# Kernel optimization log

Hardware: AMD Instinct MI355X
Metric: run time of the kernel (lower is better)

Reference implementation:

```python
import jax, jax.numpy as jnp
import numpy as np

B, S, DIM = 2, 2048, 2048
NH, HD, HDR = 16, 128, 64
DCKV, DCQ = 512, 1536


def _lin(x, W, b):
    return x @ W.T + b


def _rotate_half(x):
    x1, x2 = jnp.split(x, 2, axis=-1)
    return jnp.concatenate([-x2, x1], axis=-1)


def _rope(x, cos, sin):
    # x: [..., s, hdr]; cos/sin: [s, hdr]
    return x * cos + _rotate_half(x) * sin


def setup_inputs() -> dict:
    key = jax.random.key(0)
    ks = jax.random.split(key, 20)
    sc = 0.02

    def w(k, shape):
        return (jax.random.normal(k, shape, jnp.float32) * sc)

    inp = {}
    inp['x'] = jax.random.normal(ks[0], (B, S, DIM), jnp.float32)
    # standard RoPE tables for the decoupled rotary dim
    inv_freq = 1.0 / (10000.0 ** (jnp.arange(0, HDR, 2, dtype=jnp.float32) / HDR))
    t = jnp.arange(S, dtype=jnp.float32)
    freqs = jnp.outer(t, inv_freq)                      # [S, HDR/2]
    emb = jnp.concatenate([freqs, freqs], axis=-1)      # [S, HDR]
    inp['freq_cos'] = jnp.cos(emb)
    inp['freq_sin'] = jnp.sin(emb)
    inp['W_dq'] = w(ks[1], (DCQ, DIM));  inp['b_dq'] = jnp.zeros((DCQ,), jnp.float32)
    inp['W_uq'] = w(ks[2], (NH * HD, DCQ)); inp['b_uq'] = jnp.zeros((NH * HD,), jnp.float32)
    inp['W_qr'] = w(ks[3], (NH * HDR, DCQ)); inp['b_qr'] = jnp.zeros((NH * HDR,), jnp.float32)
    inp['W_dkv'] = w(ks[4], (DCKV, DIM)); inp['b_dkv'] = jnp.zeros((DCKV,), jnp.float32)
    inp['W_uk'] = w(ks[5], (NH * HD, DCKV)); inp['b_uk'] = jnp.zeros((NH * HD,), jnp.float32)
    inp['W_uv'] = w(ks[6], (NH * HD, DCKV)); inp['b_uv'] = jnp.zeros((NH * HD,), jnp.float32)
    inp['W_kr'] = w(ks[7], (HDR, DIM)); inp['b_kr'] = jnp.zeros((HDR,), jnp.float32)
    inp['W_out'] = w(ks[8], (DIM, DIM)); inp['b_out'] = jnp.zeros((DIM,), jnp.float32)
    return inp


def reference(x, freq_cos, freq_sin,
              W_dq, b_dq, W_uq, b_uq, W_qr, b_qr,
              W_dkv, b_dkv, W_uk, b_uk, W_uv, b_uv,
              W_kr, b_kr, W_out, b_out):
    b, s, d = x.shape
    c_q = _lin(x, W_dq, b_dq)                                  # [b,s,dcq]
    c_kv = _lin(x, W_dkv, b_dkv)                               # [b,s,dckv]
    c_q_r = _lin(c_q, W_qr, b_qr).reshape(b, s, NH, HDR).transpose(0, 2, 1, 3)  # [b,nh,s,hdr]
    k_r = _lin(x, W_kr, b_kr)[:, None]                         # [b,1,s,hdr]
    cos = freq_cos[:s]
    sin = freq_sin[:s]
    r_q = _rope(c_q_r, cos, sin)
    r_k = _rope(k_r, cos, sin)
    r_q = r_q.transpose(0, 2, 1, 3).reshape(b, s, NH * HDR)    # [b,s,nh*hdr]
    r_k = r_k[:, 0]                                            # [b,s,hdr]
    q = jnp.concatenate([_lin(c_q, W_uq, b_uq), r_q], axis=-1)  # [b,s,nh*hd+nh*hdr]
    k_base = _lin(c_kv, W_uk, b_uk)                            # [b,s,nh*hd]
    v = _lin(c_kv, W_uv, b_uv)                                 # [b,s,nh*hd]
    r_k_exp = jnp.broadcast_to(r_k[:, :, None, :], (b, s, NH, HDR)).reshape(b, s, NH * HDR)
    k = jnp.concatenate([k_base, r_k_exp], axis=-1)
    # faithful to original: view the concat into nh chunks of (hd+hdr)
    q = q.reshape(b, s, NH, HD + HDR).transpose(0, 2, 1, 3)    # [b,nh,s,hd+hdr]
    k = k.reshape(b, s, NH, HD + HDR).transpose(0, 2, 1, 3)
    v = v.reshape(b, s, NH, HD).transpose(0, 2, 1, 3)          # [b,nh,s,hd]
    scale = 1.0 / np.float32(np.sqrt(HD + HDR))
    att = jnp.einsum('bhqd,bhkd->bhqk', q, k) * scale          # [b,nh,s,s]
    mask = jnp.tril(jnp.ones((s, s), dtype=bool))
    att = jnp.where(mask, att, jnp.float32(-jnp.inf))
    att = jax.nn.softmax(att, axis=-1)
    y = jnp.einsum('bhqk,bhkd->bhqd', att, v)                  # [b,nh,s,hd]
    y = y.transpose(0, 2, 1, 3).reshape(b, s, d)
    return _lin(y, W_out, b_out)
```

## Files before the change

### kernel.cpp

```cpp
#include <hip/hip_runtime.h>
#include <hip/hip_bf16.h>
#include <stdint.h>


typedef __bf16 bf16x8 __attribute__((ext_vector_type(8)));
typedef float  f32x4  __attribute__((ext_vector_type(4)));

__device__ __forceinline__ uint16_t f2bf(float f) {
    uint32_t u = __builtin_bit_cast(uint32_t, f);
    u = (u + 0x7FFFu + ((u >> 16) & 1u)) >> 16;
    return (uint16_t)u;
}
__device__ __forceinline__ float bf2f(uint16_t h) {
    uint32_t u = ((uint32_t)h) << 16;
    return __builtin_bit_cast(float, u);
}

typedef __attribute__((address_space(3))) uint32_t lds_u32_t;
typedef const __attribute__((address_space(1))) uint32_t glb_u32_t;

__device__ __forceinline__ void gld16(const void* g, const void* l) {
    __builtin_amdgcn_global_load_lds((glb_u32_t*)(uintptr_t)g,
                                     (lds_u32_t*)(uint32_t)(uintptr_t)l, 16, 0, 0);
}

__global__ __launch_bounds__(256)
void conv_kernel(const float* __restrict__ src, uint16_t* __restrict__ dst,
                 int n_src, int n_dst)
{
    int i = (blockIdx.x * 256 + threadIdx.x) << 2;
    if (i >= n_dst) return;
    ushort4 o;
    if (i < n_src) {
        float4 v = *(const float4*)(src + i);
        o.x = f2bf(v.x); o.y = f2bf(v.y); o.z = f2bf(v.z); o.w = f2bf(v.w);
    } else {
        o.x = 0; o.y = 0; o.z = 0; o.w = 0;
    }
    *(ushort4*)(dst + i) = o;
}

template<int MODE>
__global__ __launch_bounds__(256, 2)
void gemm_fused(const uint16_t* __restrict__ A, const uint16_t* __restrict__ W,
                const float* __restrict__ b0, const float* __restrict__ b1,
                const float* __restrict__ b2,
                void* __restrict__ O0, void* __restrict__ O1,
                int M, int N, int K, int lda, int s1, int s2)
{
    __shared__ __align__(16) uint16_t Alds[128 * 32];
    __shared__ __align__(16) uint16_t Blds[128 * 32];

    const int tid  = threadIdx.x;
    const int lane = tid & 63;
    const int wave = tid >> 6;
    const int wm   = wave >> 1;
    const int wn   = wave & 1;
    const int m0   = blockIdx.y << 7;
    const int n0   = blockIdx.x << 7;

    f32x4 acc[4][4];
    #pragma unroll
    for (int i = 0; i < 4; ++i)
        #pragma unroll
        for (int j = 0; j < 4; ++j)
            acc[i][j] = (f32x4){0.f, 0.f, 0.f, 0.f};

    const int r0 = (wave << 5) + (lane >> 2);
    const int ck = (lane & 3) << 3;
    const uint16_t* gA0 = A + (size_t)(m0 + r0) * lda + ck;
    const uint16_t* gA1 = gA0 + (size_t)16 * lda;
    const uint16_t* gB0 = W + (size_t)(n0 + r0) * K + ck;
    const uint16_t* gB1 = gB0 + (size_t)16 * K;
    const uint16_t* lA0 = Alds + (wave << 10);
    const uint16_t* lA1 = lA0 + 512;
    const uint16_t* lB0 = Blds + (wave << 10);
    const uint16_t* lB1 = lB0 + 512;

    const int rsel = lane & 15;
    const int g8   = (lane >> 4) << 3;

    const int nK = K >> 5;
    for (int kt = 0; kt < nK; ++kt) {
        __syncthreads();
        gld16(gA0, lA0); gld16(gA1, lA1);
        gld16(gB0, lB0); gld16(gB1, lB1);
        gA0 += 32; gA1 += 32; gB0 += 32; gB1 += 32;
        __syncthreads();

        bf16x8 af[4], bfr[4];
        #pragma unroll
        for (int i = 0; i < 4; ++i)
            af[i] = *(const bf16x8*)&Alds[(((wm << 6) + (i << 4) + rsel) << 5) + g8];
        #pragma unroll
        for (int j = 0; j < 4; ++j)
            bfr[j] = *(const bf16x8*)&Blds[(((wn << 6) + (j << 4) + rsel) << 5) + g8];

        #pragma unroll
        for (int i = 0; i < 4; ++i)
            #pragma unroll
            for (int j = 0; j < 4; ++j)
                acc[i][j] = __builtin_amdgcn_mfma_f32_16x16x32_bf16(af[i], bfr[j], acc[i][j], 0, 0, 0);
    }

    const int col = lane & 15;
    const int rg  = lane >> 4;
    #pragma unroll
    for (int i = 0; i < 4; ++i) {
        #pragma unroll
        for (int j = 0; j < 4; ++j) {
            int n = n0 + (wn << 6) + (j << 4) + col;
            if (n >= N) continue;
            float bv = (n < s1) ? b0[n] : (n < s2) ? b1[n - s1] : b2[n - s2];
            float v[4];
            #pragma unroll
            for (int r = 0; r < 4; ++r) v[r] = acc[i][j][r] + bv;
            int mbase = m0 + (wm << 6) + (i << 4) + (rg << 2);
            if (MODE == 0) {
                uint16_t* o = (uint16_t*)O0 + (size_t)mbase * N + n;
                #pragma unroll
                for (int r = 0; r < 4; ++r) o[(size_t)r * N] = f2bf(v[r]);
            } else if (MODE == 3) {
                float* o = (float*)O0 + (size_t)mbase * N + n;
                #pragma unroll
                for (int r = 0; r < 4; ++r) o[(size_t)r * N] = v[r];
            } else {
                if (n < s1) {
                    int hh = n / 192, d = n - hh * 192;
                    int b = mbase >> 11, s = mbase & 2047;
                    uint16_t* o = (uint16_t*)O0 + (((size_t)(b * 16 + hh) * 2048 + s) * 192) + d;
                    #pragma unroll
                    for (int r = 0; r < 4; ++r) o[r * 192] = f2bf(v[r]);
                } else if (MODE == 4) {
                    int nn = n - s1;
                    uint16_t* o = (uint16_t*)O1 + (size_t)mbase * (N - s1) + nn;
                    #pragma unroll
                    for (int r = 0; r < 4; ++r) o[(size_t)r * (N - s1)] = f2bf(v[r]);
                } else {
                    int nn = n - s1;
                    int hh = nn >> 7, d = nn & 127;
                    int b = mbase >> 11, s = mbase & 2047;
                    ushort4 o4;
                    o4.x = f2bf(v[0]); o4.y = f2bf(v[1]); o4.z = f2bf(v[2]); o4.w = f2bf(v[3]);
                    *(ushort4*)&((uint16_t*)O1)[(((size_t)(b * 16 + hh) * 128 + d) * 2048) + s] = o4;
                }
            }
        }
    }
}

__global__ __launch_bounds__(256)
void rope_q_kernel(const uint16_t* __restrict__ raw, const float* __restrict__ fc,
                   const float* __restrict__ fs, uint16_t* __restrict__ qp)
{
    int gid = blockIdx.x * 256 + threadIdx.x;
    int m = gid >> 10, n = gid & 1023;
    int hh = n >> 6, d = n & 63;
    int b = m >> 11, s = m & 2047;
    float x  = bf2f(raw[(size_t)m * 1024 + n]);
    float xo = bf2f(raw[(size_t)m * 1024 + hh * 64 + ((d < 32) ? d + 32 : d - 32)]);
    float rot = (d < 32) ? -xo : xo;
    float v = x * fc[s * 64 + d] + rot * fs[s * 64 + d];
    int f = 2048 + n;
    int head = f / 192, dq = f - head * 192;
    qp[(((size_t)(b * 16 + head) * 2048 + s) * 192) + dq] = f2bf(v);
}

__global__ __launch_bounds__(256)
void rope_k_kernel(const uint16_t* __restrict__ raw, int ldr,
                   const float* __restrict__ fc, const float* __restrict__ fs,
                   uint16_t* __restrict__ kp)
{
    int gid = blockIdx.x * 256 + threadIdx.x;
    int m = gid >> 6, d = gid & 63;
    int b = m >> 11, s = m & 2047;
    float x  = bf2f(raw[(size_t)m * ldr + d]);
    float xo = bf2f(raw[(size_t)m * ldr + ((d < 32) ? d + 32 : d - 32)]);
    float rot = (d < 32) ? -xo : xo;
    uint16_t bv = f2bf(x * fc[s * 64 + d] + rot * fs[s * 64 + d]);
    #pragma unroll
    for (int hh = 0; hh < 16; ++hh) {
        int f = 2048 + hh * 64 + d;
        int head = f / 192, dk = f - head * 192;
        kp[(((size_t)(b * 16 + head) * 2048 + s) * 192) + dk] = bv;
    }
}

__global__ __launch_bounds__(256)
void attn_mfma3(const uint16_t* __restrict__ qp, const uint16_t* __restrict__ kp,
                const uint16_t* __restrict__ vt, uint16_t* __restrict__ yf)
{
    __shared__ uint16_t Ks[64][200];
    __shared__ uint16_t Vs[128][72];
    __shared__ uint16_t Ps[4][16][72];

    const int tid  = threadIdx.x;
    const int lane = tid & 63;
    const int w    = tid >> 6;
    const int g    = lane >> 4;
    const int li   = lane & 15;
    const int bh   = blockIdx.y;
    const int b    = bh >> 4;
    const int h    = bh & 15;

    const size_t qkb = (size_t)bh * 2048 * 192;
    const size_t vtb = (size_t)bh * 128 * 2048;
    const float scl = 0.07216878364870323f * 1.4426950408889634f;

    for (int pass = 0; pass < 2; ++pass) {
        const int jq = pass ? (int)blockIdx.x : 31 - (int)blockIdx.x;
        const int q0 = jq << 6;

        bf16x8 qf[6];
        #pragma unroll
        for (int kk = 0; kk < 6; ++kk)
            qf[kk] = *(const bf16x8*)(qp + qkb +
                (size_t)(q0 + (w << 4) + li) * 192 + kk * 32 + (g << 3));

        float mst[4], lst[4];
        f32x4 oacc[8];
        #pragma unroll
        for (int r = 0; r < 4; ++r) { mst[r] = -__builtin_inff(); lst[r] = 0.f; }
        #pragma unroll
        for (int ct = 0; ct < 8; ++ct) oacc[ct] = (f32x4){0.f, 0.f, 0.f, 0.f};

        for (int t = 0; t <= jq; ++t) {
            const int j0 = t << 6;
            __syncthreads();
            #pragma unroll
            for (int p = 0; p < 6; ++p) {
                int idx = tid + p * 256;
                int r = idx / 24, c8 = (idx - r * 24) << 3;
                *(bf16x8*)&Ks[r][c8] = *(const bf16x8*)(kp + qkb + (size_t)(j0 + r) * 192 + c8);
            }
            #pragma unroll
            for (int p = 0; p < 8; ++p) {
                int idx = tid + p * 256;
                int r = idx >> 4, c4 = (idx & 15) << 2;
                *(ushort4*)&Vs[r][c4] = *(const ushort4*)(vt + vtb + (size_t)r * 2048 + j0 + c4);
            }
            __syncthreads();

            f32x4 sacc[4];
            #pragma unroll
            for (int c = 0; c < 4; ++c) sacc[c] = (f32x4){0.f, 0.f, 0.f, 0.f};
            #pragma unroll
            for (int c = 0; c < 4; ++c) {
                #pragma unroll
                for (int kk = 0; kk < 6; ++kk) {
                    bf16x8 kf = *(const bf16x8*)&Ks[(c << 4) + li][kk * 32 + (g << 3)];
                    sacc[c] = __builtin_amdgcn_mfma_f32_16x16x32_bf16(qf[kk], kf, sacc[c], 0, 0, 0);
                }
            }

            float corr[4];
            #pragma unroll
            for (int r = 0; r < 4; ++r) {
                const int rq = q0 + (w << 4) + (g << 2) + r;
                float sv[4];
                float mx = -__builtin_inff();
                #pragma unroll
                for (int c = 0; c < 4; ++c) {
                    int colk = j0 + (c << 4) + li;
                    sv[c] = (colk <= rq) ? sacc[c][r] * scl : -__builtin_inff();
                    mx = fmaxf(mx, sv[c]);
                }
                #pragma unroll
                for (int off = 8; off >= 1; off >>= 1) mx = fmaxf(mx, __shfl_xor(mx, off, 64));
                float mnew = fmaxf(mst[r], mx);
                corr[r] = exp2f(mst[r] - mnew);
                mst[r] = mnew;
                float psum = 0.f;
                #pragma unroll
                for (int c = 0; c < 4; ++c) {
                    float p = exp2f(sv[c] - mnew);
                    psum += p;
                    Ps[w][(g << 2) + r][(c << 4) + li] = f2bf(p);
                }
                #pragma unroll
                for (int off = 8; off >= 1; off >>= 1) psum += __shfl_xor(psum, off, 64);
                lst[r] = lst[r] * corr[r] + psum;
            }

            #pragma unroll
            for (int ct = 0; ct < 8; ++ct)
                #pragma unroll
                for (int r = 0; r < 4; ++r) oacc[ct][r] *= corr[r];

            bf16x8 pf0 = *(const bf16x8*)&Ps[w][li][(g << 3)];
            bf16x8 pf1 = *(const bf16x8*)&Ps[w][li][32 + (g << 3)];
            #pragma unroll
            for (int ct = 0; ct < 8; ++ct) {
                bf16x8 vf0 = *(const bf16x8*)&Vs[(ct << 4) + li][(g << 3)];
                bf16x8 vf1 = *(const bf16x8*)&Vs[(ct << 4) + li][32 + (g << 3)];
                oacc[ct] = __builtin_amdgcn_mfma_f32_16x16x32_bf16(pf0, vf0, oacc[ct], 0, 0, 0);
                oacc[ct] = __builtin_amdgcn_mfma_f32_16x16x32_bf16(pf1, vf1, oacc[ct], 0, 0, 0);
            }
        }

        #pragma unroll
        for (int r = 0; r < 4; ++r) {
            float inv = 1.f / lst[r];
            int rq = q0 + (w << 4) + (g << 2) + r;
            size_t obase = ((size_t)(b * 2048 + rq) * 2048) + h * 128;
            #pragma unroll
            for (int ct = 0; ct < 8; ++ct)
                yf[obase + (ct << 4) + li] = f2bf(oacc[ct][r] * inv);
        }
    }
}

extern "C" void kernel_launch(void* const* d_in, const int* in_sizes, int n_in,
                              void* d_out, int out_size, void* d_ws, size_t ws_size,
                              hipStream_t stream)
{
    const float* x     = (const float*)d_in[0];
    const float* fcos  = (const float*)d_in[1];
    const float* fsin  = (const float*)d_in[2];
    const float* W_dq  = (const float*)d_in[3];
    const float* b_dq  = (const float*)d_in[4];
    const float* W_uq  = (const float*)d_in[5];
    const float* b_uq  = (const float*)d_in[6];
    const float* W_qr  = (const float*)d_in[7];
    const float* b_qr  = (const float*)d_in[8];
    const float* W_dkv = (const float*)d_in[9];
    const float* b_dkv = (const float*)d_in[10];
    const float* W_uk  = (const float*)d_in[11];
    const float* b_uk  = (const float*)d_in[12];
    const float* W_uv  = (const float*)d_in[13];
    const float* b_uv  = (const float*)d_in[14];
    const float* W_kr  = (const float*)d_in[15];
    const float* b_kr  = (const float*)d_in[16];
    const float* W_out = (const float*)d_in[17];
    const float* b_out = (const float*)d_in[18];

    char* ws = (char*)d_ws;
    uint16_t* xb     = (uint16_t*)(ws + 0);
    uint16_t* Wcat2  = (uint16_t*)(ws + 0);
    uint16_t* Wcat3  = (uint16_t*)(ws + 9437184);
    uint16_t* yf     = (uint16_t*)(ws + 0);
    uint16_t* Wout_b = (uint16_t*)(ws + 16777216);
    uint16_t* qp     = (uint16_t*)(ws + 25165824);
    uint16_t* kp     = (uint16_t*)(ws + 50331648);
    uint16_t* qr_raw = (uint16_t*)(ws + 50331648);
    uint16_t* vt     = (uint16_t*)(ws + 75497472);
    uint16_t* Wcat1  = (uint16_t*)(ws + 75497472);
    uint16_t* c_all  = (uint16_t*)(ws + 92274688);

    dim3 blk(256);
    conv_kernel<<<dim3(8192), blk, 0, stream>>>(x,     xb,                8388608, 8388608);
    conv_kernel<<<dim3(3072), blk, 0, stream>>>(W_dq,  Wcat1,             3145728, 3145728);
    conv_kernel<<<dim3(1024), blk, 0, stream>>>(W_dkv, Wcat1 + 3145728,   1048576, 1048576);
    conv_kernel<<<dim3( 256), blk, 0, stream>>>(W_kr,  Wcat1 + 4194304,    131072,  262144);
    conv_kernel<<<dim3(4096), blk, 0, stream>>>(W_out, Wout_b,            4194304, 4194304);

    gemm_fused<0><<<dim3(17, 32), blk, 0, stream>>>(
        xb, Wcat1, b_dq, b_dkv, b_kr, c_all, nullptr,
        4096, 2112, 2048, 2048, 1536, 2048);

    conv_kernel<<<dim3(3072), blk, 0, stream>>>(W_uq, Wcat2,             3145728, 3145728);
    conv_kernel<<<dim3(1536), blk, 0, stream>>>(W_qr, Wcat2 + 3145728,   1572864, 1572864);
    conv_kernel<<<dim3(1024), blk, 0, stream>>>(W_uk, Wcat3,             1048576, 1048576);
    conv_kernel<<<dim3(1024), blk, 0, stream>>>(W_uv, Wcat3 + 1048576,   1048576, 1048576);

    gemm_fused<4><<<dim3(24, 32), blk, 0, stream>>>(
        c_all, Wcat2, b_uq, b_qr, b_qr, qp, qr_raw,
        4096, 3072, 1536, 2112, 2048, 3072);

    rope_q_kernel<<<dim3(16384), blk, 0, stream>>>(qr_raw, fcos, fsin, qp);

    gemm_fused<5><<<dim3(32, 32), blk, 0, stream>>>(
        c_all + 1536, Wcat3, b_uk, b_uv, b_uv, kp, vt,
        4096, 4096, 512, 2112, 2048, 4096);

    rope_k_kernel<<<dim3(1024), blk, 0, stream>>>(c_all + 2048, 2112, fcos, fsin, kp);

    attn_mfma3<<<dim3(16, 32), blk, 0, stream>>>(qp, kp, vt, yf);

    gemm_fused<3><<<dim3(16, 32), blk, 0, stream>>>(
        yf, Wout_b, b_out, b_out, b_out, d_out, nullptr,
        4096, 2048, 2048, 2048, 2048, 2048);
}
```

Before: 362.2 us.

## Fuse q RoPE into up-projection epilogue and flatten attention grid to one tile per block

Applies the q rotary embedding directly in the MODE 4 GEMM epilogue, taking the partner element from the accumulator tile j^2, which removes the separate rope_q kernel and its intermediate buffer round trip. The attention kernel now launches 1024 blocks, each handling a single query tile, ordered from the longest causal tile down. Previously 512 blocks each paired a long and a short tile. This gives the scheduler finer load balancing but loses the explicit pairing, and the epilogue now does extra loads from the cos/sin tables.

```diff
diff --git a/kernel.cpp b/kernel.cpp
--- a/kernel.cpp
+++ b/kernel.cpp
@@ -45,6 +45,7 @@
 void gemm_fused(const uint16_t* __restrict__ A, const uint16_t* __restrict__ W,
                 const float* __restrict__ b0, const float* __restrict__ b1,
                 const float* __restrict__ b2,
+                const float* __restrict__ fc, const float* __restrict__ fs,
                 void* __restrict__ O0, void* __restrict__ O1,
                 int M, int N, int K, int lda, int s1, int s2)
 {
@@ -125,21 +126,30 @@
                 #pragma unroll
                 for (int r = 0; r < 4; ++r) o[(size_t)r * N] = v[r];
             } else {
+                int b = mbase >> 11, s = mbase & 2047;
                 if (n < s1) {
                     int hh = n / 192, d = n - hh * 192;
-                    int b = mbase >> 11, s = mbase & 2047;
                     uint16_t* o = (uint16_t*)O0 + (((size_t)(b * 16 + hh) * 2048 + s) * 192) + d;
                     #pragma unroll
                     for (int r = 0; r < 4; ++r) o[r * 192] = f2bf(v[r]);
                 } else if (MODE == 4) {
                     int nn = n - s1;
-                    uint16_t* o = (uint16_t*)O1 + (size_t)mbase * (N - s1) + nn;
+                    int d  = nn & 63;
+                    float bp = b1[nn ^ 32];
+                    int f = 2048 + nn;
+                    int head = f / 192, dq = f - head * 192;
+                    uint16_t* o = (uint16_t*)O0 + (((size_t)(b * 16 + head) * 2048 + s) * 192) + dq;
                     #pragma unroll
-                    for (int r = 0; r < 4; ++r) o[(size_t)r * (N - s1)] = f2bf(v[r]);
+                    for (int r = 0; r < 4; ++r) {
+                        float pv  = acc[i][j ^ 2][r] + bp;
+                        float rot = (d < 32) ? -pv : pv;
+                        int   sl  = s + r;
+                        float out = v[r] * fc[(size_t)sl * 64 + d] + rot * fs[(size_t)sl * 64 + d];
+                        o[r * 192] = f2bf(out);
+                    }
                 } else {
                     int nn = n - s1;
                     int hh = nn >> 7, d = nn & 127;
-                    int b = mbase >> 11, s = mbase & 2047;
                     ushort4 o4;
                     o4.x = f2bf(v[0]); o4.y = f2bf(v[1]); o4.z = f2bf(v[2]); o4.w = f2bf(v[3]);
                     *(ushort4*)&((uint16_t*)O1)[(((size_t)(b * 16 + hh) * 128 + d) * 2048) + s] = o4;
@@ -147,23 +157,6 @@
             }
         }
     }
-}
-
-__global__ __launch_bounds__(256)
-void rope_q_kernel(const uint16_t* __restrict__ raw, const float* __restrict__ fc,
-                   const float* __restrict__ fs, uint16_t* __restrict__ qp)
-{
-    int gid = blockIdx.x * 256 + threadIdx.x;
-    int m = gid >> 10, n = gid & 1023;
-    int hh = n >> 6, d = n & 63;
-    int b = m >> 11, s = m & 2047;
-    float x  = bf2f(raw[(size_t)m * 1024 + n]);
-    float xo = bf2f(raw[(size_t)m * 1024 + hh * 64 + ((d < 32) ? d + 32 : d - 32)]);
-    float rot = (d < 32) ? -xo : xo;
-    float v = x * fc[s * 64 + d] + rot * fs[s * 64 + d];
-    int f = 2048 + n;
-    int head = f / 192, dq = f - head * 192;
-    qp[(((size_t)(b * 16 + head) * 2048 + s) * 192) + dq] = f2bf(v);
 }
 
 __global__ __launch_bounds__(256)
@@ -187,7 +180,7 @@
 }
 
 __global__ __launch_bounds__(256)
-void attn_mfma3(const uint16_t* __restrict__ qp, const uint16_t* __restrict__ kp,
+void attn_mfma5(const uint16_t* __restrict__ qp, const uint16_t* __restrict__ kp,
                 const uint16_t* __restrict__ vt, uint16_t* __restrict__ yf)
 {
     __shared__ uint16_t Ks[64][200];
@@ -199,114 +192,112 @@
     const int w    = tid >> 6;
     const int g    = lane >> 4;
     const int li   = lane & 15;
-    const int bh   = blockIdx.y;
+    const int idx  = blockIdx.x;
+    const int qt   = 31 - (idx >> 5);
+    const int bh   = idx & 31;
     const int b    = bh >> 4;
     const int h    = bh & 15;
+    const int q0   = qt << 6;
 
     const size_t qkb = (size_t)bh * 2048 * 192;
     const size_t vtb = (size_t)bh * 128 * 2048;
     const float scl = 0.07216878364870323f * 1.4426950408889634f;
 
-    for (int pass = 0; pass < 2; ++pass) {
-        const int jq = pass ? (int)blockIdx.x : 31 - (int)blockIdx.x;
-        const int q0 = jq << 6;
-
-        bf16x8 qf[6];
-        #pragma unroll
-        for (int kk = 0; kk < 6; ++kk)
-            qf[kk] = *(const bf16x8*)(qp + qkb +
-                (size_t)(q0 + (w << 4) + li) * 192 + kk * 32 + (g << 3));
-
-        float mst[4], lst[4];
-        f32x4 oacc[8];
-        #pragma unroll
-        for (int r = 0; r < 4; ++r) { mst[r] = -__builtin_inff(); lst[r] = 0.f; }
-        #pragma unroll
-        for (int ct = 0; ct < 8; ++ct) oacc[ct] = (f32x4){0.f, 0.f, 0.f, 0.f};
-
-        for (int t = 0; t <= jq; ++t) {
-            const int j0 = t << 6;
-            __syncthreads();
-            #pragma unroll
-            for (int p = 0; p < 6; ++p) {
-                int idx = tid + p * 256;
-                int r = idx / 24, c8 = (idx - r * 24) << 3;
-                *(bf16x8*)&Ks[r][c8] = *(const bf16x8*)(kp + qkb + (size_t)(j0 + r) * 192 + c8);
+    bf16x8 qf[6];
+    #pragma unroll
+    for (int kk = 0; kk < 6; ++kk)
+        qf[kk] = *(const bf16x8*)(qp + qkb +
+            (size_t)(q0 + (w << 4) + li) * 192 + kk * 32 + (g << 3));
+
+    float mst[4], lst[4];
+    f32x4 oacc[8];
+    #pragma unroll
+    for (int r = 0; r < 4; ++r) { mst[r] = -__builtin_inff(); lst[r] = 0.f; }
+    #pragma unroll
+    for (int ct = 0; ct < 8; ++ct) oacc[ct] = (f32x4){0.f, 0.f, 0.f, 0.f};
+
+    for (int t = 0; t <= qt; ++t) {
+        const int j0 = t << 6;
+        __syncthreads();
+        #pragma unroll
+        for (int p = 0; p < 6; ++p) {
+            int idx2 = tid + p * 256;
+            int r = idx2 / 24, c8 = (idx2 - r * 24) << 3;
+            *(bf16x8*)&Ks[r][c8] = *(const bf16x8*)(kp + qkb + (size_t)(j0 + r) * 192 + c8);
+        }
+        #pragma unroll
+        for (int p = 0; p < 8; ++p) {
+            int idx2 = tid + p * 256;
+            int r = idx2 >> 4, c4 = (idx2 & 15) << 2;
+            *(ushort4*)&Vs[r][c4] = *(const ushort4*)(vt + vtb + (size_t)r * 2048 + j0 + c4);
+        }
+        __syncthreads();
+
+        f32x4 sacc[4];
+        #pragma unroll
+        for (int c = 0; c < 4; ++c) sacc[c] = (f32x4){0.f, 0.f, 0.f, 0.f};
+        #pragma unroll
+        for (int c = 0; c < 4; ++c) {
+            #pragma unroll
+            for (int kk = 0; kk < 6; ++kk) {
+                bf16x8 kf = *(const bf16x8*)&Ks[(c << 4) + li][kk * 32 + (g << 3)];
+                sacc[c] = __builtin_amdgcn_mfma_f32_16x16x32_bf16(qf[kk], kf, sacc[c], 0, 0, 0);
             }
-            #pragma unroll
-            for (int p = 0; p < 8; ++p) {
-                int idx = tid + p * 256;
-                int r = idx >> 4, c4 = (idx & 15) << 2;
-                *(ushort4*)&Vs[r][c4] = *(const ushort4*)(vt + vtb + (size_t)r * 2048 + j0 + c4);
+        }
+
+        float corr[4];
+        #pragma unroll
+        for (int r = 0; r < 4; ++r) {
+            const int rq = q0 + (w << 4) + (g << 2) + r;
+            float sv[4];
+            float mx = -__builtin_inff();
+            #pragma unroll
+            for (int c = 0; c < 4; ++c) {
+                int colk = j0 + (c << 4) + li;
+                sv[c] = (colk <= rq) ? sacc[c][r] * scl : -__builtin_inff();
+                mx = fmaxf(mx, sv[c]);
             }
-            __syncthreads();
-
-            f32x4 sacc[4];
-            #pragma unroll
-            for (int c = 0; c < 4; ++c) sacc[c] = (f32x4){0.f, 0.f, 0.f, 0.f};
+            #pragma unroll
+            for (int off = 8; off >= 1; off >>= 1) mx = fmaxf(mx, __shfl_xor(mx, off, 64));
+            float mnew = fmaxf(mst[r], mx);
+            corr[r] = exp2f(mst[r] - mnew);
+            mst[r] = mnew;
+            float psum = 0.f;
             #pragma unroll
             for (int c = 0; c < 4; ++c) {
-                #pragma unroll
-                for (int kk = 0; kk < 6; ++kk) {
-                    bf16x8 kf = *(const bf16x8*)&Ks[(c << 4) + li][kk * 32 + (g << 3)];
-                    sacc[c] = __builtin_amdgcn_mfma_f32_16x16x32_bf16(qf[kk], kf, sacc[c], 0, 0, 0);
-                }
+                float p = exp2f(sv[c] - mnew);
+                psum += p;
+                Ps[w][(g << 2) + r][(c << 4) + li] = f2bf(p);
             }
-
-            float corr[4];
-            #pragma unroll
-            for (int r = 0; r < 4; ++r) {
-                const int rq = q0 + (w << 4) + (g << 2) + r;
-                float sv[4];
-                float mx = -__builtin_inff();
-                #pragma unroll
-                for (int c = 0; c < 4; ++c) {
-                    int colk = j0 + (c << 4) + li;
-                    sv[c] = (colk <= rq) ? sacc[c][r] * scl : -__builtin_inff();
-                    mx = fmaxf(mx, sv[c]);
-                }
-                #pragma unroll
-                for (int off = 8; off >= 1; off >>= 1) mx = fmaxf(mx, __shfl_xor(mx, off, 64));
-                float mnew = fmaxf(mst[r], mx);
-                corr[r] = exp2f(mst[r] - mnew);
-                mst[r] = mnew;
-                float psum = 0.f;
-                #pragma unroll
-                for (int c = 0; c < 4; ++c) {
-                    float p = exp2f(sv[c] - mnew);
-                    psum += p;
-                    Ps[w][(g << 2) + r][(c << 4) + li] = f2bf(p);
-                }
-                #pragma unroll
-                for (int off = 8; off >= 1; off >>= 1) psum += __shfl_xor(psum, off, 64);
-                lst[r] = lst[r] * corr[r] + psum;
-            }
-
-            #pragma unroll
-            for (int ct = 0; ct < 8; ++ct)
-                #pragma unroll
-                for (int r = 0; r < 4; ++r) oacc[ct][r] *= corr[r];
-
-            bf16x8 pf0 = *(const bf16x8*)&Ps[w][li][(g << 3)];
-            bf16x8 pf1 = *(const bf16x8*)&Ps[w][li][32 + (g << 3)];
-            #pragma unroll
-            for (int ct = 0; ct < 8; ++ct) {
-                bf16x8 vf0 = *(const bf16x8*)&Vs[(ct << 4) + li][(g << 3)];
-                bf16x8 vf1 = *(const bf16x8*)&Vs[(ct << 4) + li][32 + (g << 3)];
-                oacc[ct] = __builtin_amdgcn_mfma_f32_16x16x32_bf16(pf0, vf0, oacc[ct], 0, 0, 0);
-                oacc[ct] = __builtin_amdgcn_mfma_f32_16x16x32_bf16(pf1, vf1, oacc[ct], 0, 0, 0);
-            }
-        }
-
-        #pragma unroll
-        for (int r = 0; r < 4; ++r) {
-            float inv = 1.f / lst[r];
-            int rq = q0 + (w << 4) + (g << 2) + r;
-            size_t obase = ((size_t)(b * 2048 + rq) * 2048) + h * 128;
-            #pragma unroll
-            for (int ct = 0; ct < 8; ++ct)
-                yf[obase + (ct << 4) + li] = f2bf(oacc[ct][r] * inv);
-        }
+            #pragma unroll
+            for (int off = 8; off >= 1; off >>= 1) psum += __shfl_xor(psum, off, 64);
+            lst[r] = lst[r] * corr[r] + psum;
+        }
+
+        #pragma unroll
+        for (int ct = 0; ct < 8; ++ct)
+            #pragma unroll
+            for (int r = 0; r < 4; ++r) oacc[ct][r] *= corr[r];
+
+        bf16x8 pf0 = *(const bf16x8*)&Ps[w][li][(g << 3)];
+        bf16x8 pf1 = *(const bf16x8*)&Ps[w][li][32 + (g << 3)];
+        #pragma unroll
+        for (int ct = 0; ct < 8; ++ct) {
+            bf16x8 vf0 = *(const bf16x8*)&Vs[(ct << 4) + li][(g << 3)];
+            bf16x8 vf1 = *(const bf16x8*)&Vs[(ct << 4) + li][32 + (g << 3)];
+            oacc[ct] = __builtin_amdgcn_mfma_f32_16x16x32_bf16(pf0, vf0, oacc[ct], 0, 0, 0);
+            oacc[ct] = __builtin_amdgcn_mfma_f32_16x16x32_bf16(pf1, vf1, oacc[ct], 0, 0, 0);
+        }
+    }
+
+    #pragma unroll
+    for (int r = 0; r < 4; ++r) {
+        float inv = 1.f / lst[r];
+        int rq = q0 + (w << 4) + (g << 2) + r;
+        size_t obase = ((size_t)(b * 2048 + rq) * 2048) + h * 128;
+        #pragma unroll
+        for (int ct = 0; ct < 8; ++ct)
+            yf[obase + (ct << 4) + li] = f2bf(oacc[ct][r] * inv);
     }
 }
 
@@ -342,7 +333,6 @@
     uint16_t* Wout_b = (uint16_t*)(ws + 16777216);
     uint16_t* qp     = (uint16_t*)(ws + 25165824);
     uint16_t* kp     = (uint16_t*)(ws + 50331648);
-    uint16_t* qr_raw = (uint16_t*)(ws + 50331648);
     uint16_t* vt     = (uint16_t*)(ws + 75497472);
     uint16_t* Wcat1  = (uint16_t*)(ws + 75497472);
     uint16_t* c_all  = (uint16_t*)(ws + 92274688);
@@ -355,7 +345,7 @@
     conv_kernel<<<dim3(4096), blk, 0, stream>>>(W_out, Wout_b,            4194304, 4194304);
 
     gemm_fused<0><<<dim3(17, 32), blk, 0, stream>>>(
-        xb, Wcat1, b_dq, b_dkv, b_kr, c_all, nullptr,
+        xb, Wcat1, b_dq, b_dkv, b_kr, nullptr, nullptr, c_all, nullptr,
         4096, 2112, 2048, 2048, 1536, 2048);
 
     conv_kernel<<<dim3(3072), blk, 0, stream>>>(W_uq, Wcat2,             3145728, 3145728);
@@ -364,20 +354,18 @@
     conv_kernel<<<dim3(1024), blk, 0, stream>>>(W_uv, Wcat3 + 1048576,   1048576, 1048576);
 
     gemm_fused<4><<<dim3(24, 32), blk, 0, stream>>>(
-        c_all, Wcat2, b_uq, b_qr, b_qr, qp, qr_raw,
+        c_all, Wcat2, b_uq, b_qr, b_qr, fcos, fsin, qp, nullptr,
         4096, 3072, 1536, 2112, 2048, 3072);
 
-    rope_q_kernel<<<dim3(16384), blk, 0, stream>>>(qr_raw, fcos, fsin, qp);
-
     gemm_fused<5><<<dim3(32, 32), blk, 0, stream>>>(
-        c_all + 1536, Wcat3, b_uk, b_uv, b_uv, kp, vt,
+        c_all + 1536, Wcat3, b_uk, b_uv, b_uv, nullptr, nullptr, kp, vt,
         4096, 4096, 512, 2112, 2048, 4096);
 
     rope_k_kernel<<<dim3(1024), blk, 0, stream>>>(c_all + 2048, 2112, fcos, fsin, kp);
 
-    attn_mfma3<<<dim3(16, 32), blk, 0, stream>>>(qp, kp, vt, yf);
+    attn_mfma5<<<dim3(1024), blk, 0, stream>>>(qp, kp, vt, yf);
 
     gemm_fused<3><<<dim3(16, 32), blk, 0, stream>>>(
-        yf, Wout_b, b_out, b_out, b_out, d_out, nullptr,
+        yf, Wout_b, b_out, b_out, b_out, nullptr, nullptr, d_out, nullptr,
         4096, 2048, 2048, 2048, 2048, 2048);
 }
```

Result: no change. 357.4 us (-1.3%).
